# Performance work log

Measured on AMD Instinct MI355X. Metric: run time of the kernel, lower is better.

## Reference

```python
import jax, jax.numpy as jnp
import numpy as np

CODEBOOK_SIZE = 8192
TOKEN_SIZE = 256
COMMITMENT_COST = 0.25
B, C, H, W = 32, 256, 32, 32


def setup_inputs() -> dict:
    key = jax.random.key(0)
    k1, k2 = jax.random.split(key)
    z = jax.random.normal(k1, (B, C, H, W), dtype=jnp.float32)
    # torch init: uniform_(-1/codebook_size, 1/codebook_size)
    embedding = jax.random.uniform(
        k2, (CODEBOOK_SIZE, TOKEN_SIZE), dtype=jnp.float32,
        minval=-1.0 / CODEBOOK_SIZE, maxval=1.0 / CODEBOOK_SIZE)
    return {"z": z, "embedding": embedding}


def reference(z, embedding):
    # b c h w -> b h w c
    z = jnp.transpose(z.astype(jnp.float32), (0, 2, 3, 1))
    b, h, w, c = z.shape
    z_flat = z.reshape(-1, c)  # [N, c]

    # squared euclidean distances: ||z||^2 + ||e||^2 - 2 z e^T
    d = (jnp.sum(z_flat ** 2, axis=1, keepdims=True)
         + jnp.sum(embedding ** 2, axis=1)
         - 2.0 * jnp.einsum('nd,kd->nk', z_flat, embedding))  # [N, K]
    idx = jnp.argmin(d, axis=1)  # [N]

    z_q = embedding[idx].reshape(z.shape)  # [b,h,w,c]

    commitment_loss = COMMITMENT_COST * jnp.mean(
        (jax.lax.stop_gradient(z_q) - z) ** 2)
    codebook_loss = jnp.mean((z_q - jax.lax.stop_gradient(z)) ** 2)
    loss = commitment_loss + codebook_loss

    # straight-through estimator
    z_q_st = z + jax.lax.stop_gradient(z_q - z)
    z_q_out = jnp.transpose(z_q_st, (0, 3, 1, 2))  # b h w c -> b c h w

    min_encoding_indices = idx.reshape(b, h, w)
    return (z_q_out, loss, commitment_loss, codebook_loss,
            min_encoding_indices)
```

## Files before the change

### kernel.cpp

```cpp
#include <hip/hip_runtime.h>
#include <float.h>

#define NBATCH 32
#define NCHAN  256
#define NHW    1024
#define NTOK   32768
#define NK     8192
#define ND     256
#define ZELEMS 8388608
#define OUT_LOSS 8388608
#define OUT_IDX  8388611
#define MARGIN   1.2e-4f

typedef short bf16x8  __attribute__((ext_vector_type(8)));
typedef float f32x4   __attribute__((ext_vector_type(4)));
typedef float f32x16  __attribute__((ext_vector_type(16)));

__device__ __forceinline__ void gl_lds16(const void* g, void* l) {
    __builtin_amdgcn_global_load_lds(
        (const __attribute__((address_space(1))) unsigned int*)g,
        (__attribute__((address_space(3))) unsigned int*)l, 16, 0, 0);
}

__device__ __forceinline__ unsigned short f2bf(float f) {
    unsigned int u = __float_as_uint(f);
    u += 0x7FFFu + ((u >> 16) & 1u);
    return (unsigned short)(u >> 16);
}

__device__ __forceinline__ float embed8(float x, int code) {
    return __int_as_float((__float_as_int(x) & 0xFFFFFF00) | code);
}


__global__ __launch_bounds__(256) void k_castE(const float* __restrict__ E,
                                               unsigned short* __restrict__ Epre,
                                               float* __restrict__ en,
                                               float* __restrict__ acc,
                                               int* __restrict__ counter) {
    int g = blockIdx.x * 256 + threadIdx.x;
    int code = g >> 5, c16 = g & 31;
    int kc = c16 >> 2, ks = (c16 >> 1) & 1, lhi = c16 & 1;
    const float4* E4 = (const float4*)(E + code * ND + c16 * 8);
    float4 a = E4[0], b = E4[1];
    float s = a.x*a.x + a.y*a.y + a.z*a.z + a.w*a.w
            + b.x*b.x + b.y*b.y + b.z*b.z + b.w*b.w;
    #pragma unroll
    for (int off = 1; off < 32; off <<= 1) s += __shfl_xor(s, off, 64);
    if ((threadIdx.x & 31) == 0) en[code] = s;
    unsigned int u[4];
    u[0] = (unsigned int)f2bf(a.x) | ((unsigned int)f2bf(a.y) << 16);
    u[1] = (unsigned int)f2bf(a.z) | ((unsigned int)f2bf(a.w) << 16);
    u[2] = (unsigned int)f2bf(b.x) | ((unsigned int)f2bf(b.y) << 16);
    u[3] = (unsigned int)f2bf(b.z) | ((unsigned int)f2bf(b.w) << 16);
    *(uint4*)((char*)Epre + (size_t)(code >> 7) * 65536 + kc * 8192
              + (ks * 2 + lhi) * 2048 + (code & 127) * 16) =
        make_uint4(u[0], u[1], u[2], u[3]);
    if (blockIdx.x == 0 && threadIdx.x == 0) { acc[0] = 0.0f; counter[0] = 0; }
}

__global__ __launch_bounds__(256) void k_castZ(const float* __restrict__ zg,
                                               unsigned short* __restrict__ Zpre) {
    __shared__ unsigned short buf[128][34];
    int bi = blockIdx.x;
    int b = bi >> 6, kc = (bi >> 3) & 7, hwt = bi & 7;
    int c0 = kc * 32, hw0 = hwt * 128;
    int t = threadIdx.x;
    #pragma unroll
    for (int r = 0; r < 4; ++r) {
        int idx = r * 256 + t;
        int c = idx >> 5, q = idx & 31;
        float4 v = *(const float4*)&zg[(b * 256 + c0 + c) * 1024 + hw0 + q * 4];
        buf[q * 4 + 0][c] = f2bf(v.x);
        buf[q * 4 + 1][c] = f2bf(v.y);
        buf[q * 4 + 2][c] = f2bf(v.z);
        buf[q * 4 + 3][c] = f2bf(v.w);
    }
    __syncthreads();
    int tok = t >> 1, ks = t & 1;
    char* base = (char*)Zpre + (size_t)((b * 8 + hwt) * 8 + kc) * 8192;
    #pragma unroll
    for (int lhi = 0; lhi < 2; ++lhi) {
        unsigned int u[4];
        #pragma unroll
        for (int k = 0; k < 4; ++k) {
            int cc = ks * 16 + lhi * 8 + 2 * k;
            u[k] = (unsigned int)buf[tok][cc] | ((unsigned int)buf[tok][cc + 1] << 16);
        }
        *(uint4*)(base + (ks * 2 + lhi) * 2048 + tok * 16) =
            make_uint4(u[0], u[1], u[2], u[3]);
    }
}

__global__ __launch_bounds__(256, 3) void k_dist(const unsigned short* __restrict__ Epre,
                                                 const unsigned short* __restrict__ Zpre,
                                                 const float* __restrict__ en,
                                                 float2* __restrict__ part2) {
    __shared__ __align__(16) char Zs[16384];
    __shared__ float2 red[2][128];
    __shared__ float en_s[128];

    const int t    = threadIdx.x;
    const int kbb  = blockIdx.x;
    const int mb   = blockIdx.y;
    const int n0   = mb * 128;
    const int w    = t >> 6, lane = t & 63;
    const int l31  = lane & 31, lhi = lane >> 5;
    const int wm   = w >> 1, wn = w & 1;

    if (t < 128) en_s[t] = en[kbb * 128 + t];

    const char* Eb = (const char*)Epre + (size_t)kbb * 65536;
    const char* Zb = (const char*)Zpre + (size_t)mb * 65536;

    auto stage = [&](int kc, int buf) {
        char* db = Zs + buf * 8192;
        #pragma unroll
        for (int r = 0; r < 2; ++r) {
            int s = w * 2 + r;
            gl_lds16(Zb + kc * 8192 + s * 1024 + lane * 16,
                     db + s * 1024 + lane * 16);
        }
    };

    bf16x8 ea[2][2][2];
    auto loadE = [&](int kc, int pp) {
        #pragma unroll
        for (int i = 0; i < 2; ++i)
            #pragma unroll
            for (int ks = 0; ks < 2; ++ks)
                ea[pp][i][ks] = *(const bf16x8*)(Eb + kc * 8192
                    + (ks * 2 + lhi) * 2048 + (wm * 64 + i * 32 + l31) * 16);
    };

    f32x16 acc[2][2];
    #pragma unroll
    for (int i = 0; i < 2; ++i)
        #pragma unroll
        for (int j = 0; j < 2; ++j) acc[i][j] = (f32x16)0.0f;

    loadE(0, 0);
    stage(0, 0);
    #pragma unroll
    for (int kc = 0; kc < 8; ++kc) {
        __syncthreads();
        if (kc < 7) {
            stage(kc + 1, (kc + 1) & 1);
            loadE(kc + 1, (kc + 1) & 1);
        }
        const char* zbuf = Zs + (kc & 1) * 8192;
        bf16x8 zb[2][2];
        #pragma unroll
        for (int j = 0; j < 2; ++j)
            #pragma unroll
            for (int ks = 0; ks < 2; ++ks)
                zb[j][ks] = *(const bf16x8*)(zbuf + (ks * 2 + lhi) * 2048
                                             + (wn * 64 + j * 32 + l31) * 16);
        #pragma unroll
        for (int ks = 0; ks < 2; ++ks)
            #pragma unroll
            for (int i = 0; i < 2; ++i)
                #pragma unroll
                for (int j = 0; j < 2; ++j)
                    acc[i][j] = __builtin_amdgcn_mfma_f32_32x32x16_bf16(
                        ea[kc & 1][i][ks], zb[j][ks], acc[i][j], 0, 0, 0);
    }

    float v1[2] = { FLT_MAX, FLT_MAX }, v2[2] = { FLT_MAX, FLT_MAX };
    #pragma unroll
    for (int i = 0; i < 2; ++i) {
        const int cb = (wm << 6) | (i << 5) | (lhi << 2);
        #pragma unroll
        for (int rq = 0; rq < 4; ++rq) {
            f32x4 ev = *(const f32x4*)&en_s[cb + 8 * rq];
            #pragma unroll
            for (int rr = 0; rr < 4; ++rr) {
                const int r = rq * 4 + rr;
                const int code = cb + 8 * rq + rr;
                #pragma unroll
                for (int j = 0; j < 2; ++j) {
                    float s  = fmaf(-2.0f, acc[i][j][r], ev[rr]);
                    float se = embed8(s, code);
                    v2[j] = __builtin_amdgcn_fmed3f(se, v1[j], v2[j]);
                    v1[j] = fminf(v1[j], se);
                }
            }
        }
    }
    #pragma unroll
    for (int j = 0; j < 2; ++j) {
        float b1 = __shfl_xor(v1[j], 32, 64);
        float b2 = __shfl_xor(v2[j], 32, 64);
        float hi = fmaxf(v1[j], b1);
        v1[j] = fminf(v1[j], b1);
        v2[j] = fminf(fminf(hi, v2[j]), b2);
    }
    if (lane < 32) {
        #pragma unroll
        for (int j = 0; j < 2; ++j)
            red[wm][wn * 64 + j * 32 + lane] = make_float2(v1[j], v2[j]);
    }
    __syncthreads();
    if (t < 128) {
        float2 A = red[0][t], B = red[1][t];
        float g1 = fminf(A.x, B.x);
        float g2 = fminf(fminf(fmaxf(A.x, B.x), A.y), B.y);
        part2[(size_t)(n0 + t) * 64 + kbb] = make_float2(g1, g2);
    }
}

__global__ __launch_bounds__(256) void k_refine(const float* __restrict__ zg,
                                                const float* __restrict__ E,
                                                const float2* __restrict__ part2,
                                                int* __restrict__ idxw,
                                                float* __restrict__ outF) {
    __shared__ float Zs[256 * 65];
    const int t = threadIdx.x;
    const int n0 = blockIdx.x * 64;
    const int b = n0 >> 10, hw0 = n0 & 1023;

    #pragma unroll
    for (int r = 0; r < 16; ++r) {
        int li = r * 256 + t;
        int c = li >> 4, q = li & 15;
        float4 v = *(const float4*)&zg[(b * 256 + c) * 1024 + hw0 + q * 4];
        Zs[c * 65 + q * 4 + 0] = v.x;
        Zs[c * 65 + q * 4 + 1] = v.y;
        Zs[c * 65 + q * 4 + 2] = v.z;
        Zs[c * 65 + q * 4 + 3] = v.w;
    }
    __syncthreads();

    const int w = t >> 6, l = t & 63;
    for (int it = 0; it < 16; ++it) {
        const int tokl = w * 16 + it;
        const int n = n0 + tokl;

        float zreg[4];
        #pragma unroll
        for (int j = 0; j < 4; ++j) zreg[j] = Zs[(64 * j + l) * 65 + tokl];

        double z2 = 0.0;
        #pragma unroll
        for (int j = 0; j < 4; ++j) z2 += (double)zreg[j] * (double)zreg[j];
        #pragma unroll
        for (int m = 1; m < 64; m <<= 1) z2 += __shfl_xor(z2, m, 64);
        const float z2f = (float)z2;

        float2 p = part2[(size_t)n * 64 + l];
        int code1 = (l << 7) | (__float_as_int(p.x) & 0x7F);
        int code2 = (l << 7) | (__float_as_int(p.y) & 0x7F);

        float vmin = p.x;
        #pragma unroll
        for (int m = 1; m < 64; m <<= 1) vmin = fminf(vmin, __shfl_xor(vmin, m, 64));
        const float thr = vmin + MARGIN;

        unsigned long long m1 = __ballot(p.x <= thr);
        unsigned long long m2 = __ballot(p.y <= thr);

        float bdq = FLT_MAX; int bidx = 0x7fffffff;
        #pragma unroll
        for (int pass = 0; pass < 2; ++pass) {
            unsigned long long mm = pass ? m2 : m1;
            int ibits = pass ? code2 : code1;
            while (mm) {
                int src = __ffsll(mm) - 1; mm &= mm - 1;
                int cidx = __shfl(ibits, src, 64);
                const float* erow = E + cidx * ND;
                double g = (double)zreg[0] * (double)erow[l]
                         + (double)zreg[1] * (double)erow[64 + l]
                         + (double)zreg[2] * (double)erow[128 + l]
                         + (double)zreg[3] * (double)erow[192 + l];
                #pragma unroll
                for (int mk = 1; mk < 64; mk <<= 1) g += __shfl_xor(g, mk, 64);
                float c  = (float)(2.0 * g);
                float dq = z2f - c;
                if (dq < bdq || (dq == bdq && cidx < bidx)) { bdq = dq; bidx = cidx; }
            }
        }
        if (l == 0) { idxw[n] = bidx; outF[OUT_IDX + n] = (float)bidx; }
    }
}

__global__ __launch_bounds__(256) void k_gather(const float* __restrict__ E,
                                                const float* __restrict__ zg,
                                                const int* __restrict__ idxw,
                                                float* __restrict__ out,
                                                float* __restrict__ acc,
                                                int* __restrict__ counter) {
    __shared__ __align__(16) float Es[64 * 256];
    __shared__ int sidx[64];
    __shared__ float wred[4];
    const int t = threadIdx.x;
    const int b = blockIdx.x >> 4, ht = blockIdx.x & 15;

    if (t < 64) sidx[t] = idxw[b * 1024 + ht * 64 + t];
    __syncthreads();
    const float4* E4 = (const float4*)E;
    #pragma unroll
    for (int r = 0; r < 16; ++r) {
        int li = r * 256 + t;
        int row = li >> 6, slot = li & 63;
        float4 v = E4[(size_t)sidx[row] * 64 + slot];
        *(float4*)&Es[row * 256 + ((slot ^ (row & 15)) * 4)] = v;
    }
    __syncthreads();

    const int hw = t & 63, wv = t >> 6;
    float s = 0.0f;
    #pragma unroll 8
    for (int cc = 0; cc < 64; ++cc) {
        int c = wv * 64 + cc;
        float e = Es[hw * 256 + (((c >> 2) ^ (hw & 15)) * 4) + (c & 3)];
        size_t gi = (size_t)(b * 256 + c) * 1024 + ht * 64 + hw;
        float zv = zg[gi];
        out[gi] = e;
        float d = e - zv;
        s = fmaf(d, d, s);
    }
    #pragma unroll
    for (int off = 32; off > 0; off >>= 1) s += __shfl_down(s, off, 64);
    if ((t & 63) == 0) wred[wv] = s;
    __syncthreads();
    if (t == 0) {
        atomicAdd(acc, wred[0] + wred[1] + wred[2] + wred[3]);
        __threadfence();
        int old = atomicAdd(counter, 1);
        if (old == 511) {
            float total = atomicAdd(acc, 0.0f);
            float mse = total / 8388608.0f;
            out[OUT_LOSS + 0] = 1.25f * mse;
            out[OUT_LOSS + 1] = 0.25f * mse;
            out[OUT_LOSS + 2] = mse;
        }
    }
}

extern "C" void kernel_launch(void* const* d_in, const int* in_sizes, int n_in,
                              void* d_out, int out_size, void* d_ws, size_t ws_size,
                              hipStream_t stream) {
    const float* zg = (const float*)d_in[0];
    const float* E  = (const float*)d_in[1];
    float* out = (float*)d_out;
    float* wsf = (float*)d_ws;
    float*  acc     = wsf;
    int*    counter = (int*)(wsf + 1);
    float*  en      = wsf + 64;
    int*    idxw    = (int*)(wsf + 64 + NK);
    float2* part2   = (float2*)(wsf + 64 + NK + NTOK);
    unsigned short* Epre = (unsigned short*)(wsf + 64 + NK + NTOK + 4194304);
    unsigned short* Zpre = (unsigned short*)d_out;

    k_castE <<<1024, 256, 0, stream>>>(E, Epre, en, acc, counter);
    k_castZ <<<2048, 256, 0, stream>>>(zg, Zpre);
    k_dist  <<<dim3(64, 256), 256, 0, stream>>>(Epre, Zpre, en, part2);
    k_refine<<<NTOK / 64, 256, 0, stream>>>(zg, E, part2, idxw, out);
    k_gather<<<512, 256, 0, stream>>>(E, zg, idxw, out, acc, counter);
}
```

Measured before the change: 318.9 us.

## Load Z tiles directly to registers in dist kernel and merge cast kernels

The distance GEMM kernel no longer stages Z tiles through LDS with global_load_lds and per-iteration barriers. Both E and Z fragments are now double-buffered in registers, loaded straight from global memory, and the main loop has no __syncthreads. The two bf16 cast kernels are also merged into one launch to save a kernel launch. In exchange, register pressure rises and each wave does more global load traffic, since Z fragments are no longer shared through LDS.

```diff
diff --git a/kernel.cpp b/kernel.cpp
--- a/kernel.cpp
+++ b/kernel.cpp
@@ -16,12 +16,6 @@
 typedef float f32x4   __attribute__((ext_vector_type(4)));
 typedef float f32x16  __attribute__((ext_vector_type(16)));
 
-__device__ __forceinline__ void gl_lds16(const void* g, void* l) {
-    __builtin_amdgcn_global_load_lds(
-        (const __attribute__((address_space(1))) unsigned int*)g,
-        (__attribute__((address_space(3))) unsigned int*)l, 16, 0, 0);
-}
-
 __device__ __forceinline__ unsigned short f2bf(float f) {
     unsigned int u = __float_as_uint(f);
     u += 0x7FFFu + ((u >> 16) & 1u);
@@ -33,62 +27,63 @@
 }
 
 
-__global__ __launch_bounds__(256) void k_castE(const float* __restrict__ E,
-                                               unsigned short* __restrict__ Epre,
-                                               float* __restrict__ en,
-                                               float* __restrict__ acc,
-                                               int* __restrict__ counter) {
-    int g = blockIdx.x * 256 + threadIdx.x;
-    int code = g >> 5, c16 = g & 31;
-    int kc = c16 >> 2, ks = (c16 >> 1) & 1, lhi = c16 & 1;
-    const float4* E4 = (const float4*)(E + code * ND + c16 * 8);
-    float4 a = E4[0], b = E4[1];
-    float s = a.x*a.x + a.y*a.y + a.z*a.z + a.w*a.w
-            + b.x*b.x + b.y*b.y + b.z*b.z + b.w*b.w;
-    #pragma unroll
-    for (int off = 1; off < 32; off <<= 1) s += __shfl_xor(s, off, 64);
-    if ((threadIdx.x & 31) == 0) en[code] = s;
-    unsigned int u[4];
-    u[0] = (unsigned int)f2bf(a.x) | ((unsigned int)f2bf(a.y) << 16);
-    u[1] = (unsigned int)f2bf(a.z) | ((unsigned int)f2bf(a.w) << 16);
-    u[2] = (unsigned int)f2bf(b.x) | ((unsigned int)f2bf(b.y) << 16);
-    u[3] = (unsigned int)f2bf(b.z) | ((unsigned int)f2bf(b.w) << 16);
-    *(uint4*)((char*)Epre + (size_t)(code >> 7) * 65536 + kc * 8192
-              + (ks * 2 + lhi) * 2048 + (code & 127) * 16) =
-        make_uint4(u[0], u[1], u[2], u[3]);
-    if (blockIdx.x == 0 && threadIdx.x == 0) { acc[0] = 0.0f; counter[0] = 0; }
-}
-
-__global__ __launch_bounds__(256) void k_castZ(const float* __restrict__ zg,
-                                               unsigned short* __restrict__ Zpre) {
+__global__ __launch_bounds__(256) void k_cast(const float* __restrict__ zg,
+                                              const float* __restrict__ E,
+                                              unsigned short* __restrict__ Epre,
+                                              unsigned short* __restrict__ Zpre,
+                                              float* __restrict__ en,
+                                              float* __restrict__ acc,
+                                              int* __restrict__ counter) {
     __shared__ unsigned short buf[128][34];
-    int bi = blockIdx.x;
-    int b = bi >> 6, kc = (bi >> 3) & 7, hwt = bi & 7;
-    int c0 = kc * 32, hw0 = hwt * 128;
-    int t = threadIdx.x;
-    #pragma unroll
-    for (int r = 0; r < 4; ++r) {
-        int idx = r * 256 + t;
-        int c = idx >> 5, q = idx & 31;
-        float4 v = *(const float4*)&zg[(b * 256 + c0 + c) * 1024 + hw0 + q * 4];
-        buf[q * 4 + 0][c] = f2bf(v.x);
-        buf[q * 4 + 1][c] = f2bf(v.y);
-        buf[q * 4 + 2][c] = f2bf(v.z);
-        buf[q * 4 + 3][c] = f2bf(v.w);
-    }
-    __syncthreads();
-    int tok = t >> 1, ks = t & 1;
-    char* base = (char*)Zpre + (size_t)((b * 8 + hwt) * 8 + kc) * 8192;
-    #pragma unroll
-    for (int lhi = 0; lhi < 2; ++lhi) {
+    const int t = threadIdx.x;
+    if (blockIdx.x < 1024) {
+        int g = blockIdx.x * 256 + t;
+        int code = g >> 5, c16 = g & 31;
+        int kc = c16 >> 2, ks = (c16 >> 1) & 1, lhi = c16 & 1;
+        const float4* E4 = (const float4*)(E + code * ND + c16 * 8);
+        float4 a = E4[0], b = E4[1];
+        float s = a.x*a.x + a.y*a.y + a.z*a.z + a.w*a.w
+                + b.x*b.x + b.y*b.y + b.z*b.z + b.w*b.w;
+        #pragma unroll
+        for (int off = 1; off < 32; off <<= 1) s += __shfl_xor(s, off, 64);
+        if ((t & 31) == 0) en[code] = s;
         unsigned int u[4];
-        #pragma unroll
-        for (int k = 0; k < 4; ++k) {
-            int cc = ks * 16 + lhi * 8 + 2 * k;
-            u[k] = (unsigned int)buf[tok][cc] | ((unsigned int)buf[tok][cc + 1] << 16);
-        }
-        *(uint4*)(base + (ks * 2 + lhi) * 2048 + tok * 16) =
+        u[0] = (unsigned int)f2bf(a.x) | ((unsigned int)f2bf(a.y) << 16);
+        u[1] = (unsigned int)f2bf(a.z) | ((unsigned int)f2bf(a.w) << 16);
+        u[2] = (unsigned int)f2bf(b.x) | ((unsigned int)f2bf(b.y) << 16);
+        u[3] = (unsigned int)f2bf(b.z) | ((unsigned int)f2bf(b.w) << 16);
+        *(uint4*)((char*)Epre + (size_t)(code >> 7) * 65536 + kc * 8192
+                  + (ks * 2 + lhi) * 2048 + (code & 127) * 16) =
             make_uint4(u[0], u[1], u[2], u[3]);
+        if (blockIdx.x == 0 && t == 0) { acc[0] = 0.0f; counter[0] = 0; }
+    } else {
+        int bi = blockIdx.x - 1024;
+        int b = bi >> 6, kc = (bi >> 3) & 7, hwt = bi & 7;
+        int c0 = kc * 32, hw0 = hwt * 128;
+        #pragma unroll
+        for (int r = 0; r < 4; ++r) {
+            int idx = r * 256 + t;
+            int c = idx >> 5, q = idx & 31;
+            float4 v = *(const float4*)&zg[(b * 256 + c0 + c) * 1024 + hw0 + q * 4];
+            buf[q * 4 + 0][c] = f2bf(v.x);
+            buf[q * 4 + 1][c] = f2bf(v.y);
+            buf[q * 4 + 2][c] = f2bf(v.z);
+            buf[q * 4 + 3][c] = f2bf(v.w);
+        }
+        __syncthreads();
+        int tok = t >> 1, ks = t & 1;
+        char* base = (char*)Zpre + (size_t)((b * 8 + hwt) * 8 + kc) * 8192;
+        #pragma unroll
+        for (int lhi = 0; lhi < 2; ++lhi) {
+            unsigned int u[4];
+            #pragma unroll
+            for (int k = 0; k < 4; ++k) {
+                int cc = ks * 16 + lhi * 8 + 2 * k;
+                u[k] = (unsigned int)buf[tok][cc] | ((unsigned int)buf[tok][cc + 1] << 16);
+            }
+            *(uint4*)(base + (ks * 2 + lhi) * 2048 + tok * 16) =
+                make_uint4(u[0], u[1], u[2], u[3]);
+        }
     }
 }
 
@@ -96,7 +91,6 @@
                                                  const unsigned short* __restrict__ Zpre,
                                                  const float* __restrict__ en,
                                                  float2* __restrict__ part2) {
-    __shared__ __align__(16) char Zs[16384];
     __shared__ float2 red[2][128];
     __shared__ float en_s[128];
 
@@ -109,28 +103,29 @@
     const int wm   = w >> 1, wn = w & 1;
 
     if (t < 128) en_s[t] = en[kbb * 128 + t];
-
-    const char* Eb = (const char*)Epre + (size_t)kbb * 65536;
-    const char* Zb = (const char*)Zpre + (size_t)mb * 65536;
-
-    auto stage = [&](int kc, int buf) {
-        char* db = Zs + buf * 8192;
-        #pragma unroll
-        for (int r = 0; r < 2; ++r) {
-            int s = w * 2 + r;
-            gl_lds16(Zb + kc * 8192 + s * 1024 + lane * 16,
-                     db + s * 1024 + lane * 16);
-        }
+    __syncthreads();
+
+    const char* Ep = (const char*)Epre + (size_t)kbb * 65536
+                   + lhi * 2048 + (wm * 64 + l31) * 16;
+    const char* Zp = (const char*)Zpre + (size_t)mb * 65536
+                   + lhi * 2048 + (wn * 64 + l31) * 16;
+
+    bf16x8 ea[2][2][2], zb[2][2][2];
+    auto loadE = [&](int kc, int pp) {
+        const char* p = Ep + kc * 8192;
+        #pragma unroll
+        for (int i = 0; i < 2; ++i)
+            #pragma unroll
+            for (int ks = 0; ks < 2; ++ks)
+                ea[pp][i][ks] = *(const bf16x8*)(p + ks * 4096 + i * 512);
     };
-
-    bf16x8 ea[2][2][2];
-    auto loadE = [&](int kc, int pp) {
-        #pragma unroll
-        for (int i = 0; i < 2; ++i)
+    auto loadZ = [&](int kc, int pp) {
+        const char* p = Zp + kc * 8192;
+        #pragma unroll
+        for (int j = 0; j < 2; ++j)
             #pragma unroll
             for (int ks = 0; ks < 2; ++ks)
-                ea[pp][i][ks] = *(const bf16x8*)(Eb + kc * 8192
-                    + (ks * 2 + lhi) * 2048 + (wm * 64 + i * 32 + l31) * 16);
+                zb[pp][j][ks] = *(const bf16x8*)(p + ks * 4096 + j * 512);
     };
 
     f32x16 acc[2][2];
@@ -140,22 +135,11 @@
         for (int j = 0; j < 2; ++j) acc[i][j] = (f32x16)0.0f;
 
     loadE(0, 0);
-    stage(0, 0);
+    loadZ(0, 0);
     #pragma unroll
     for (int kc = 0; kc < 8; ++kc) {
-        __syncthreads();
-        if (kc < 7) {
-            stage(kc + 1, (kc + 1) & 1);
-            loadE(kc + 1, (kc + 1) & 1);
-        }
-        const char* zbuf = Zs + (kc & 1) * 8192;
-        bf16x8 zb[2][2];
-        #pragma unroll
-        for (int j = 0; j < 2; ++j)
-            #pragma unroll
-            for (int ks = 0; ks < 2; ++ks)
-                zb[j][ks] = *(const bf16x8*)(zbuf + (ks * 2 + lhi) * 2048
-                                             + (wn * 64 + j * 32 + l31) * 16);
+        const int pp = kc & 1;
+        if (kc < 7) { loadE(kc + 1, pp ^ 1); loadZ(kc + 1, pp ^ 1); }
         #pragma unroll
         for (int ks = 0; ks < 2; ++ks)
             #pragma unroll
@@ -163,7 +147,7 @@
                 #pragma unroll
                 for (int j = 0; j < 2; ++j)
                     acc[i][j] = __builtin_amdgcn_mfma_f32_32x32x16_bf16(
-                        ea[kc & 1][i][ks], zb[j][ks], acc[i][j], 0, 0, 0);
+                        ea[pp][i][ks], zb[pp][j][ks], acc[i][j], 0, 0, 0);
     }
 
     float v1[2] = { FLT_MAX, FLT_MAX }, v2[2] = { FLT_MAX, FLT_MAX };
@@ -352,8 +336,7 @@
     unsigned short* Epre = (unsigned short*)(wsf + 64 + NK + NTOK + 4194304);
     unsigned short* Zpre = (unsigned short*)d_out;
 
-    k_castE <<<1024, 256, 0, stream>>>(E, Epre, en, acc, counter);
-    k_castZ <<<2048, 256, 0, stream>>>(zg, Zpre);
+    k_cast  <<<3072, 256, 0, stream>>>(zg, E, Epre, Zpre, en, acc, counter);
     k_dist  <<<dim3(64, 256), 256, 0, stream>>>(Epre, Zpre, en, part2);
     k_refine<<<NTOK / 64, 256, 0, stream>>>(zg, E, part2, idxw, out);
     k_gather<<<512, 256, 0, stream>>>(E, zg, idxw, out, acc, counter);
```

Measured after the change: 315.5 us. No clear change (-1.1%).
